# Kernel optimization log

Hardware: AMD Instinct MI355X
Metric: run time of the kernel (lower is better)

## Reference

```python
import jax, jax.numpy as jnp
import numpy as np

T = 1_500_000   # traindata rows
N = 2_000_000   # neighbor rows
n = 1_048_576   # layer's n (divisible by 4)
m = 1           # layer's m (sort column)
NEG_INIT = -100000.0


def setup_inputs() -> dict:
    key = jax.random.key(0)
    k1, k2, k3, k4, k5 = jax.random.split(key, 5)
    feats = jax.random.normal(k1, (T, 3), dtype=jnp.float32)
    # col 0: node ID = arange(T); cols 1:4: features
    traindata = jnp.concatenate([jnp.arange(T, dtype=jnp.float32)[:, None], feats], axis=1)
    ids = jax.random.randint(k2, (N,), 0, T).astype(jnp.float32)      # col 0: IDs into traindata
    sortcol = jax.random.normal(k3, (N,), dtype=jnp.float32)          # col m=1: sort key
    mid = jax.random.normal(k4, (N, 2), dtype=jnp.float32)            # cols 2,3
    flag = jax.random.randint(k5, (N,), 0, 10).astype(jnp.float32)
    neighbor = jnp.stack([ids, sortcol, mid[:, 0], mid[:, 1], flag], axis=1)
    return {"traindata": traindata, "neighbor": neighbor}


def reference(traindata, neighbor):
    # tf.nn.top_k(bt, k=full, sorted=True) == stable descending sort
    bt = neighbor[:, m]
    order = jnp.argsort(-bt)          # stable -> ties keep original index order, like top_k
    data = neighbor[order]
    new_neighbor = data[neighbor.shape[0] - n:]   # bottom-n rows [n, 5]

    # rows of new_neighbor whose flag (col 4) == 0: append their IDs, gathered from the
    # ORIGINAL neighbor col 0 (as in the source), padded with 3 zero feature cols.
    zero_mask = new_neighbor[:, 4] == 0
    idx = jnp.nonzero(zero_mask, size=n, fill_value=0)[0]        # static-size for jit
    valid = jnp.arange(n) < jnp.sum(zero_mask)
    rev_ids = jnp.where(valid, neighbor[idx, 0], jnp.float32(-1.0))  # -1 never matches a real ID
    rev = jnp.concatenate([rev_ids[:, None], jnp.zeros((n, 3), neighbor.dtype)], axis=1)
    td = jnp.concatenate([traindata, rev], axis=0)               # [T+n, 4]
    tdlist = td[:, 0]

    # tp[e] = FIRST index where tdlist == new_neighbor[e, 0]
    # stable argsort + searchsorted(left) gives the smallest original index among equals
    sort_idx = jnp.argsort(tdlist)
    sv = tdlist[sort_idx]
    pos = jnp.searchsorted(sv, new_neighbor[:, 0], side='left')
    tp = sort_idx[pos]                                           # [n]

    max_ = jnp.max(td[tp, 1:], axis=1)                           # [n] row-wise feature max
    flags = new_neighbor[:, 4]

    G = n // 4
    tp_g = tp.reshape(G, 4)
    max_g = max_.reshape(G, 4)
    flag_g = flags.reshape(G, 4)

    # sequential 4-step recurrence per group (mirrors the j-loop with tf.cond):
    # update iff (flag != 0) == (max_ > maxmin)
    maxmin = jnp.full((G,), NEG_INIT, dtype=max_.dtype)
    maxindex = jnp.full((G,), -100, dtype=tp.dtype)
    for j in range(4):
        re1 = flag_g[:, j] != 0
        gt = max_g[:, j] > maxmin
        re = re1 == gt
        maxmin = jnp.where(re, max_g[:, j], maxmin)
        maxindex = jnp.where(re, tp_g[:, j], maxindex)

    # gather surviving traindata rows (clip guards the never-updated -100 sentinel,
    # which would be an error in the original TF graph)
    out = td[jnp.clip(maxindex, 0, td.shape[0] - 1)]             # [G, 4]
    return out
```

## Files before the change

### kernel.cpp

```cpp
#include <hip/hip_runtime.h>
#include <stdint.h>

#define T_ROWS 1500000
#define N_ROWS 2000000
#define N_SEL  1048576
#define G_CNT  (N_SEL/4)
#define LB     (N_ROWS - N_SEL)
#define TILE   4096
#define NBLK   ((N_ROWS + TILE - 1)/TILE)
#define NBLK1  (NBLK + 1)
#define THREADS 512
#define WAVES  8
#define WTILE  (TILE/WAVES)
#define WROUNDS (WTILE/64)
#define BINS   256
#define NB_MX  ((T_ROWS + THREADS - 1)/THREADS)

static_assert((uint64_t)NBLK * TILE >= N_ROWS, "tile coverage");
static_assert(T_ROWS < (1 << 21), "tp fits 21 bits");
static_assert((LB * 4) % 16 == 0, "finalize uint4 alignment");

__global__ __launch_bounds__(THREADS) void build_all(
        const float* __restrict__ nb, const float* __restrict__ td,
        uint64_t* __restrict__ codes, float* __restrict__ mxtab,
        uint32_t* __restrict__ gH) {
    const int b = blockIdx.x;
    if (b >= NBLK) {
        int i = (b - NBLK) * THREADS + threadIdx.x;
        if (i < T_ROWS) {
            float4 r = *(const float4*)(td + (size_t)i * 4);
            mxtab[i] = fmaxf(r.y, fmaxf(r.z, r.w));
        }
        return;
    }
    __shared__ uint32_t h[BINS];
    const int t = threadIdx.x;
    const int lane = t & 63;
    if (t < BINS) h[t] = 0;
    __syncthreads();
    const int base = b * TILE;
    #pragma unroll
    for (int r = 0; r < TILE / THREADS; ++r) {
        int i = base + r * THREADS + t;
        bool active = (i < N_ROWS);
        uint32_t kd = 0;
        if (active) {
            const float* row = nb + (size_t)i * 5;
            uint32_t u = __float_as_uint(row[1]);
            uint32_t ku = (u & 0x80000000u) ? ~u : (u | 0x80000000u);
            kd = ~ku;
            uint32_t tp = (uint32_t)(int)row[0];
            uint32_t fl = (row[4] != 0.0f) ? 1u : 0u;
            codes[i] = ((uint64_t)kd << 32) | (fl << 21) | tp;
        }
        uint32_t d = kd & (BINS - 1);
        uint64_t m = __ballot(active ? 1 : 0);
        #pragma unroll
        for (int bb = 0; bb < 8; ++bb) {
            uint64_t x = __ballot((active && ((d >> bb) & 1u)) ? 1 : 0);
            m = ((d >> bb) & 1u) ? (m & x) : (m & ~x);
        }
        int ldr = __ffsll((unsigned long long)m) - 1;
        if (active && lane == ldr) atomicAdd(&h[d], (uint32_t)__popcll(m));
    }
    __syncthreads();
    if (t < BINS) gH[(size_t)t * NBLK1 + b] = h[t];
}

template <int SHIFT>
__global__ __launch_bounds__(THREADS) void radix_hist(
        const uint64_t* __restrict__ src, uint32_t* __restrict__ gH) {
    __shared__ uint32_t h[BINS];
    const int t = threadIdx.x;
    const int lane = t & 63;
    if (t < BINS) h[t] = 0;
    __syncthreads();
    const int base = blockIdx.x * TILE;
    #pragma unroll
    for (int r = 0; r < TILE / THREADS; ++r) {
        int i = base + r * THREADS + t;
        bool active = (i < N_ROWS);
        uint32_t d = active ? ((uint32_t)(src[i] >> SHIFT) & (BINS - 1)) : 0u;
        uint64_t m = __ballot(active ? 1 : 0);
        #pragma unroll
        for (int bb = 0; bb < 8; ++bb) {
            uint64_t x = __ballot((active && ((d >> bb) & 1u)) ? 1 : 0);
            m = ((d >> bb) & 1u) ? (m & x) : (m & ~x);
        }
        int ldr = __ffsll((unsigned long long)m) - 1;
        if (active && lane == ldr) atomicAdd(&h[d], (uint32_t)__popcll(m));
    }
    __syncthreads();
    if (t < BINS) gH[(size_t)t * NBLK1 + blockIdx.x] = h[t];
}

__global__ void radix_rowscan(uint32_t* __restrict__ gH, uint32_t* __restrict__ totals) {
    const int d = blockIdx.x;
    const int lane = threadIdx.x;
    uint32_t* row = gH + (size_t)d * NBLK1;
    uint32_t carry = 0;
    for (int b0 = 0; b0 < NBLK; b0 += 64) {
        int i = b0 + lane;
        uint32_t v = (i < NBLK) ? row[i] : 0u;
        uint32_t s = v;
        for (int off = 1; off < 64; off <<= 1) {
            uint32_t tt = __shfl_up(s, off, 64);
            if (lane >= off) s += tt;
        }
        if (i < NBLK) row[i] = s - v + carry;
        carry += __shfl(s, 63, 64);
    }
    if (lane == 0) {
        row[NBLK] = carry;
        totals[d] = carry;
    }
}

template <int SHIFT, bool LAST>
__global__ __launch_bounds__(THREADS) void radix_scatter(
        const uint64_t* __restrict__ src, uint64_t* __restrict__ dst,
        uint32_t* __restrict__ dst32,
        const uint32_t* __restrict__ gH, const uint32_t* __restrict__ totals) {
    __shared__ uint64_t tileS[TILE];
    __shared__ uint32_t cnt32[BINS * WAVES];
    __shared__ uint32_t writeBase[BINS];
    __shared__ uint32_t lstart[BINS];
    const int t = threadIdx.x;
    const int lane = t & 63;
    const int w = t >> 6;
    const int blk = blockIdx.x;
    const int base = blk * TILE;
    const int tileCount = (N_ROWS - base < TILE) ? (N_ROWS - base) : TILE;

    #pragma unroll
    for (int k = t; k < BINS * WAVES; k += THREADS) cnt32[k] = 0u;
    __syncthreads();

    uint64_t creg[WROUNDS];
    uint32_t meta[WROUNDS];
    const uint64_t below = (lane == 0) ? 0ull : (~0ull >> (64 - lane));
    #pragma unroll
    for (int r = 0; r < WROUNDS; ++r) {
        int idx = base + w * WTILE + r * 64 + lane;
        bool active = (idx < N_ROWS);
        uint64_t c = active ? src[idx] : 0ull;
        creg[r] = c;
        uint32_t d = (uint32_t)(c >> SHIFT) & (BINS - 1);
        uint64_t m = __ballot(active ? 1 : 0);
        #pragma unroll
        for (int bb = 0; bb < 8; ++bb) {
            uint64_t x = __ballot((active && ((d >> bb) & 1u)) ? 1 : 0);
            m = ((d >> bb) & 1u) ? (m & x) : (m & ~x);
        }
        int ldr = __ffsll((unsigned long long)m) - 1;
        uint32_t cnt = (uint32_t)__popcll(m);
        uint32_t rank = (uint32_t)__popcll(m & below);
        meta[r] = rank | ((uint32_t)(ldr < 0 ? 0 : ldr) << 8) | (cnt << 16);
        if (active && lane == ldr)
            atomicAdd(&cnt32[d * WAVES + w], cnt);
    }
    __syncthreads();

    if (t < 64) {
        uint32_t tot[4], rp[4], lc[4];
        uint32_t sumT = 0, sumL = 0;
        #pragma unroll
        for (int k = 0; k < 4; ++k) {
            int d = t * 4 + k;
            tot[k] = totals[d];
            rp[k] = gH[(size_t)d * NBLK1 + blk];
            lc[k] = gH[(size_t)d * NBLK1 + blk + 1] - rp[k];
            sumT += tot[k]; sumL += lc[k];
        }
        uint32_t sT = sumT, sL = sumL;
        for (int off = 1; off < 64; off <<= 1) {
            uint32_t aT = __shfl_up(sT, off, 64);
            uint32_t aL = __shfl_up(sL, off, 64);
            if (t >= off) { sT += aT; sL += aL; }
        }
        uint32_t exT = sT - sumT, exL = sL - sumL;
        #pragma unroll
        for (int k = 0; k < 4; ++k) {
            int d = t * 4 + k;
            writeBase[d] = exT + rp[k] - exL;
            lstart[d] = exL;
            exT += tot[k]; exL += lc[k];
        }
    }
    __syncthreads();

    if (t < BINS) {
        uint32_t run = lstart[t];
        #pragma unroll
        for (int wv = 0; wv < WAVES; ++wv) {
            uint32_t c0 = cnt32[t * WAVES + wv];
            cnt32[t * WAVES + wv] = run;
            run += c0;
        }
    }
    __syncthreads();

    #pragma unroll
    for (int r = 0; r < WROUNDS; ++r) {
        int idx = base + w * WTILE + r * 64 + lane;
        bool active = (idx < N_ROWS);
        uint64_t c = creg[r];
        uint32_t d = (uint32_t)(c >> SHIFT) & (BINS - 1);
        uint32_t mt = meta[r];
        uint32_t rank = mt & 0xFFu;
        int ldr = (int)((mt >> 8) & 0xFFu);
        uint32_t cnt = mt >> 16;
        uint32_t before = 0;
        if (active && lane == ldr)
            before = atomicAdd(&cnt32[d * WAVES + w], cnt);
        before = __shfl(before, ldr, 64);
        if (active) tileS[before + rank] = c;
    }
    __syncthreads();

    #pragma unroll
    for (int r = 0; r < TILE / THREADS; ++r) {
        int p = r * THREADS + t;
        if (p < tileCount) {
            uint64_t c = tileS[p];
            uint32_t d = (uint32_t)(c >> SHIFT) & (BINS - 1);
            uint32_t g = writeBase[d] + p;
            if (!LAST) {
                dst[(size_t)g] = c;
            } else if (g >= LB) {
                dst32[g] = (uint32_t)c;
            }
        }
    }
}

__global__ void finalize(const uint32_t* __restrict__ pay, const float* __restrict__ td,
                         const float* __restrict__ mxtab, float* __restrict__ out) {
    int g = blockIdx.x * 256 + threadIdx.x;
    if (g >= G_CNT) return;
    uint4 p4 = *(const uint4*)(pay + LB + (size_t)g * 4);
    uint32_t cs[4] = {p4.x, p4.y, p4.z, p4.w};
    float maxmin = -100000.0f;
    int maxindex = -100;
    #pragma unroll
    for (int j = 0; j < 4; ++j) {
        int tp = (int)(cs[j] & 0x1FFFFFu);
        bool re1 = ((cs[j] >> 21) & 1u) != 0u;
        float mx = mxtab[tp];
        bool gt = (mx > maxmin);
        if (re1 == gt) { maxmin = mx; maxindex = tp; }
    }
    int mi = maxindex < 0 ? 0 : maxindex;
    float4 row = *(const float4*)(td + (size_t)mi * 4);
    *(float4*)(out + (size_t)g * 4) = row;
}

extern "C" void kernel_launch(void* const* d_in, const int* in_sizes, int n_in,
                              void* d_out, int out_size, void* d_ws, size_t ws_size,
                              hipStream_t stream) {
    const float* td = (const float*)d_in[0];
    const float* nb = (const float*)d_in[1];
    float* out = (float*)d_out;
    uint8_t* ws = (uint8_t*)d_ws;

    float*    mxtab  = (float*)(ws);
    uint32_t* gH     = (uint32_t*)(ws + (size_t)6 * 1024 * 1024);
    uint32_t* totals = (uint32_t*)(ws + (size_t)7 * 1024 * 1024);
    uint64_t* A      = (uint64_t*)(ws + (size_t)8 * 1024 * 1024);
    uint64_t* B      = (uint64_t*)(ws + (size_t)24 * 1024 * 1024);

    build_all<<<NBLK + NB_MX, THREADS, 0, stream>>>(nb, td, A, mxtab, gH);

    radix_rowscan<<<BINS, 64, 0, stream>>>(gH, totals);
    radix_scatter<32, false><<<NBLK, THREADS, 0, stream>>>(A, B, nullptr, gH, totals);

    radix_hist<40><<<NBLK, THREADS, 0, stream>>>(B, gH);
    radix_rowscan<<<BINS, 64, 0, stream>>>(gH, totals);
    radix_scatter<40, false><<<NBLK, THREADS, 0, stream>>>(B, A, nullptr, gH, totals);

    radix_hist<48><<<NBLK, THREADS, 0, stream>>>(A, gH);
    radix_rowscan<<<BINS, 64, 0, stream>>>(gH, totals);
    radix_scatter<48, false><<<NBLK, THREADS, 0, stream>>>(A, B, nullptr, gH, totals);

    radix_hist<56><<<NBLK, THREADS, 0, stream>>>(B, gH);
    radix_rowscan<<<BINS, 64, 0, stream>>>(gH, totals);
    radix_scatter<56, true><<<NBLK, THREADS, 0, stream>>>(B, nullptr, (uint32_t*)A, gH, totals);

    finalize<<<(G_CNT + 255) / 256, 256, 0, stream>>>((const uint32_t*)A, td, mxtab, out);
}
```

Measured before the change: 138.9 us.

## Fold radix rowscan into scatter blocks and read only key high words

Removes the separate per-digit row-scan kernel. Each scatter block now sums its own histogram row prefix and the bin totals directly from the unscanned gH, with a padded row stride for aligned vector loads. A block-wide scan over bins replaces the old single-wave scan. The histogram kernels also read only the upper 32-bit half of each key. This drops four kernel launches and their serialization, at the cost of every scatter block redundantly reading all NBLK entries for each of 256 bins.

```diff
diff --git a/kernel.cpp b/kernel.cpp
--- a/kernel.cpp
+++ b/kernel.cpp
@@ -8,7 +8,7 @@
 #define LB     (N_ROWS - N_SEL)
 #define TILE   4096
 #define NBLK   ((N_ROWS + TILE - 1)/TILE)
-#define NBLK1  (NBLK + 1)
+#define GSTR   512
 #define THREADS 512
 #define WAVES  8
 #define WTILE  (TILE/WAVES)
@@ -19,6 +19,7 @@
 static_assert((uint64_t)NBLK * TILE >= N_ROWS, "tile coverage");
 static_assert(T_ROWS < (1 << 21), "tp fits 21 bits");
 static_assert((LB * 4) % 16 == 0, "finalize uint4 alignment");
+static_assert(NBLK <= GSTR, "gH row stride");
 
 __global__ __launch_bounds__(THREADS) void build_all(
         const float* __restrict__ nb, const float* __restrict__ td,
@@ -64,10 +65,10 @@
         if (active && lane == ldr) atomicAdd(&h[d], (uint32_t)__popcll(m));
     }
     __syncthreads();
-    if (t < BINS) gH[(size_t)t * NBLK1 + b] = h[t];
-}
-
-template <int SHIFT>
+    if (t < BINS) gH[(size_t)t * GSTR + b] = h[t];
+}
+
+template <int SHIFT32>
 __global__ __launch_bounds__(THREADS) void radix_hist(
         const uint64_t* __restrict__ src, uint32_t* __restrict__ gH) {
     __shared__ uint32_t h[BINS];
@@ -76,11 +77,13 @@
     if (t < BINS) h[t] = 0;
     __syncthreads();
     const int base = blockIdx.x * TILE;
+    const uint32_t* s32 = (const uint32_t*)src;
     #pragma unroll
     for (int r = 0; r < TILE / THREADS; ++r) {
         int i = base + r * THREADS + t;
         bool active = (i < N_ROWS);
-        uint32_t d = active ? ((uint32_t)(src[i] >> SHIFT) & (BINS - 1)) : 0u;
+        uint32_t d = 0;
+        if (active) d = (s32[2 * (size_t)i + 1] >> SHIFT32) & (BINS - 1);
         uint64_t m = __ballot(active ? 1 : 0);
         #pragma unroll
         for (int bb = 0; bb < 8; ++bb) {
@@ -91,40 +94,17 @@
         if (active && lane == ldr) atomicAdd(&h[d], (uint32_t)__popcll(m));
     }
     __syncthreads();
-    if (t < BINS) gH[(size_t)t * NBLK1 + blockIdx.x] = h[t];
-}
-
-__global__ void radix_rowscan(uint32_t* __restrict__ gH, uint32_t* __restrict__ totals) {
-    const int d = blockIdx.x;
-    const int lane = threadIdx.x;
-    uint32_t* row = gH + (size_t)d * NBLK1;
-    uint32_t carry = 0;
-    for (int b0 = 0; b0 < NBLK; b0 += 64) {
-        int i = b0 + lane;
-        uint32_t v = (i < NBLK) ? row[i] : 0u;
-        uint32_t s = v;
-        for (int off = 1; off < 64; off <<= 1) {
-            uint32_t tt = __shfl_up(s, off, 64);
-            if (lane >= off) s += tt;
-        }
-        if (i < NBLK) row[i] = s - v + carry;
-        carry += __shfl(s, 63, 64);
-    }
-    if (lane == 0) {
-        row[NBLK] = carry;
-        totals[d] = carry;
-    }
+    if (t < BINS) gH[(size_t)t * GSTR + blockIdx.x] = h[t];
 }
 
 template <int SHIFT, bool LAST>
 __global__ __launch_bounds__(THREADS) void radix_scatter(
         const uint64_t* __restrict__ src, uint64_t* __restrict__ dst,
-        uint32_t* __restrict__ dst32,
-        const uint32_t* __restrict__ gH, const uint32_t* __restrict__ totals) {
+        uint32_t* __restrict__ dst32, const uint32_t* __restrict__ gH) {
     __shared__ uint64_t tileS[TILE];
     __shared__ uint32_t cnt32[BINS * WAVES];
     __shared__ uint32_t writeBase[BINS];
-    __shared__ uint32_t lstart[BINS];
+    __shared__ uint32_t wpT[WAVES], wpL[WAVES];
     const int t = threadIdx.x;
     const int lane = t & 63;
     const int w = t >> 6;
@@ -159,38 +139,48 @@
         if (active && lane == ldr)
             atomicAdd(&cnt32[d * WAVES + w], cnt);
     }
-    __syncthreads();
-
-    if (t < 64) {
-        uint32_t tot[4], rp[4], lc[4];
-        uint32_t sumT = 0, sumL = 0;
-        #pragma unroll
-        for (int k = 0; k < 4; ++k) {
-            int d = t * 4 + k;
-            tot[k] = totals[d];
-            rp[k] = gH[(size_t)d * NBLK1 + blk];
-            lc[k] = gH[(size_t)d * NBLK1 + blk + 1] - rp[k];
-            sumT += tot[k]; sumL += lc[k];
-        }
-        uint32_t sT = sumT, sL = sumL;
-        for (int off = 1; off < 64; off <<= 1) {
-            uint32_t aT = __shfl_up(sT, off, 64);
-            uint32_t aL = __shfl_up(sL, off, 64);
-            if (t >= off) { sT += aT; sL += aL; }
-        }
-        uint32_t exT = sT - sumT, exL = sL - sumL;
-        #pragma unroll
-        for (int k = 0; k < 4; ++k) {
-            int d = t * 4 + k;
-            writeBase[d] = exT + rp[k] - exL;
-            lstart[d] = exL;
-            exT += tot[k]; exL += lc[k];
-        }
-    }
-    __syncthreads();
-
+
+    uint32_t rp = 0, tot = 0, lc = 0;
     if (t < BINS) {
-        uint32_t run = lstart[t];
+        const uint32_t* row = gH + (size_t)t * GSTR;
+        lc = row[blk];
+        int i = 0;
+        for (; i + 4 <= (NBLK & ~3); i += 4) {
+            uint4 v = *(const uint4*)(row + i);
+            uint32_t s4 = v.x + v.y + v.z + v.w;
+            tot += s4;
+            if (i + 4 <= blk) rp += s4;
+            else {
+                if (i + 0 < blk) rp += v.x;
+                if (i + 1 < blk) rp += v.y;
+                if (i + 2 < blk) rp += v.z;
+                if (i + 3 < blk) rp += v.w;
+            }
+        }
+        for (; i < NBLK; ++i) {
+            uint32_t v = row[i];
+            tot += v;
+            if (i < blk) rp += v;
+        }
+    }
+    __syncthreads();
+
+    uint32_t sT = tot, sL = lc;
+    #pragma unroll
+    for (int off = 1; off < 64; off <<= 1) {
+        uint32_t aT = __shfl_up(sT, off, 64);
+        uint32_t aL = __shfl_up(sL, off, 64);
+        if (lane >= off) { sT += aT; sL += aL; }
+    }
+    if (lane == 63) { wpT[w] = sT; wpL[w] = sL; }
+    __syncthreads();
+    uint32_t exT = sT - tot, exL = sL - lc;
+    #pragma unroll
+    for (int wv = 0; wv < WAVES; ++wv) if (wv < w) { exT += wpT[wv]; exL += wpL[wv]; }
+
+    if (t < BINS) {
+        writeBase[t] = exT + rp - exL;
+        uint32_t run = exL;
         #pragma unroll
         for (int wv = 0; wv < WAVES; ++wv) {
             uint32_t c0 = cnt32[t * WAVES + wv];
@@ -263,28 +253,23 @@
     float* out = (float*)d_out;
     uint8_t* ws = (uint8_t*)d_ws;
 
-    float*    mxtab  = (float*)(ws);
-    uint32_t* gH     = (uint32_t*)(ws + (size_t)6 * 1024 * 1024);
-    uint32_t* totals = (uint32_t*)(ws + (size_t)7 * 1024 * 1024);
-    uint64_t* A      = (uint64_t*)(ws + (size_t)8 * 1024 * 1024);
-    uint64_t* B      = (uint64_t*)(ws + (size_t)24 * 1024 * 1024);
+    float*    mxtab = (float*)(ws);
+    uint32_t* gH    = (uint32_t*)(ws + (size_t)6 * 1024 * 1024);
+    uint64_t* A     = (uint64_t*)(ws + (size_t)8 * 1024 * 1024);
+    uint64_t* B     = (uint64_t*)(ws + (size_t)8 * 1024 * 1024 + 16000512);
 
     build_all<<<NBLK + NB_MX, THREADS, 0, stream>>>(nb, td, A, mxtab, gH);
 
-    radix_rowscan<<<BINS, 64, 0, stream>>>(gH, totals);
-    radix_scatter<32, false><<<NBLK, THREADS, 0, stream>>>(A, B, nullptr, gH, totals);
-
-    radix_hist<40><<<NBLK, THREADS, 0, stream>>>(B, gH);
-    radix_rowscan<<<BINS, 64, 0, stream>>>(gH, totals);
-    radix_scatter<40, false><<<NBLK, THREADS, 0, stream>>>(B, A, nullptr, gH, totals);
-
-    radix_hist<48><<<NBLK, THREADS, 0, stream>>>(A, gH);
-    radix_rowscan<<<BINS, 64, 0, stream>>>(gH, totals);
-    radix_scatter<48, false><<<NBLK, THREADS, 0, stream>>>(A, B, nullptr, gH, totals);
-
-    radix_hist<56><<<NBLK, THREADS, 0, stream>>>(B, gH);
-    radix_rowscan<<<BINS, 64, 0, stream>>>(gH, totals);
-    radix_scatter<56, true><<<NBLK, THREADS, 0, stream>>>(B, nullptr, (uint32_t*)A, gH, totals);
+    radix_scatter<32, false><<<NBLK, THREADS, 0, stream>>>(A, B, nullptr, gH);
+
+    radix_hist<8><<<NBLK, THREADS, 0, stream>>>(B, gH);
+    radix_scatter<40, false><<<NBLK, THREADS, 0, stream>>>(B, A, nullptr, gH);
+
+    radix_hist<16><<<NBLK, THREADS, 0, stream>>>(A, gH);
+    radix_scatter<48, false><<<NBLK, THREADS, 0, stream>>>(A, B, nullptr, gH);
+
+    radix_hist<24><<<NBLK, THREADS, 0, stream>>>(B, gH);
+    radix_scatter<56, true><<<NBLK, THREADS, 0, stream>>>(B, nullptr, (uint32_t*)A, gH);
 
     finalize<<<(G_CNT + 255) / 256, 256, 0, stream>>>((const uint32_t*)A, td, mxtab, out);
 }
```

After: 220.8 us. 58.9% more time.
